# Kernel optimization log

Hardware: AMD Instinct MI355X
Metric: run time of the kernel (lower is better)

The kernel has to match this reference:

```python
import jax, jax.numpy as jnp
import numpy as np

B, S, D, H = 4, 2048, 1024, 16
DEPTH = D // H  # 64


def setup_inputs() -> dict:
    key = jax.random.key(0)
    ks = jax.random.split(key, 11)
    scale = 1.0 / np.sqrt(D)
    inp = {
        "v": jax.random.normal(ks[0], (B, S, D), jnp.float32),
        "k": jax.random.normal(ks[1], (B, S, D), jnp.float32),
        "q": jax.random.normal(ks[2], (B, S, D), jnp.float32),
        # causal mask: 1.0 where attention is disallowed (strict upper triangle)
        "mask": jnp.triu(jnp.ones((S, S), jnp.float32), k=1)[None, None, :, :],
        "wq": jax.random.normal(ks[3], (D, D), jnp.float32) * scale,
        "bq": jnp.zeros((D,), jnp.float32),
        "wk": jax.random.normal(ks[4], (D, D), jnp.float32) * scale,
        "bk": jnp.zeros((D,), jnp.float32),
        "wv": jax.random.normal(ks[5], (D, D), jnp.float32) * scale,
        "bv": jnp.zeros((D,), jnp.float32),
        "wo": jax.random.normal(ks[6], (D, D), jnp.float32) * scale,
        "bo": jnp.zeros((D,), jnp.float32),
    }
    return inp


def _split_heads(x):
    # [B, S, D] -> [B, H, S, depth]
    b, s, _ = x.shape
    return x.reshape(b, s, H, DEPTH).transpose(0, 2, 1, 3)


def reference(v, k, q, mask, wq, bq, wk, bk, wv, bv, wo, bo):
    qh = _split_heads(q @ wq + bq)  # [B,H,S,depth]
    kh = _split_heads(k @ wk + bk)
    vh = _split_heads(v @ wv + bv)

    logits = jnp.einsum("bhqd,bhkd->bhqk", qh, kh) / jnp.sqrt(
        jnp.asarray(DEPTH, jnp.float32)
    )
    logits = logits + mask * -1e9
    attn = jax.nn.softmax(logits, axis=-1)  # [B,H,S,S]
    out = jnp.einsum("bhqk,bhkd->bhqd", attn, vh)
    out = out.transpose(0, 2, 1, 3).reshape(q.shape[0], -1, D)  # [B,S,D]
    return out @ wo + bo
```

## Files before the change

### kernel.cpp

```cpp
#include <hip/hip_runtime.h>

typedef _Float16 f16;
typedef _Float16 half8 __attribute__((ext_vector_type(8)));
typedef _Float16 half4v __attribute__((ext_vector_type(4)));
typedef float f32x4 __attribute__((ext_vector_type(4)));

__device__ __forceinline__ void gl_lds16(const void* g, void* l) {
    __builtin_amdgcn_global_load_lds((const __attribute__((address_space(1))) void*)g,
                                     (__attribute__((address_space(3))) void*)l, 16, 0, 0);
}

__device__ __forceinline__ void prep_w_body(const float* __restrict__ W, f16* __restrict__ Wt)
{
    __shared__ float t[64][65];
    const int tid = threadIdx.x;
    const int tk = blockIdx.x * 64, tn = blockIdx.y * 64;
    const int rr = tid >> 4, cc = (tid & 15) * 4;
    #pragma unroll
    for (int j = 0; j < 4; ++j) {
        float4 v = *(const float4*)(W + (size_t)(tk + rr + j * 16) * 1024 + tn + cc);
        t[rr + j * 16][cc] = v.x; t[rr + j * 16][cc + 1] = v.y;
        t[rr + j * 16][cc + 2] = v.z; t[rr + j * 16][cc + 3] = v.w;
    }
    __syncthreads();
    const int n = tid >> 2, kc = (tid & 3) * 16;
    f16 o[16];
    #pragma unroll
    for (int j = 0; j < 16; ++j) o[j] = (f16)t[kc + j][n];
    f16* dst = Wt + (size_t)(tn + n) * 1024 + tk + kc;
    *(uint4*)dst = *(uint4*)o;
    *(uint4*)(dst + 8) = *(uint4*)(o + 8);
}

__global__ __launch_bounds__(256) void prep_w1(const float* __restrict__ W, f16* __restrict__ Wt)
{ prep_w_body(W, Wt); }

__global__ __launch_bounds__(256) void prep_w3(const float* __restrict__ w0,
    const float* __restrict__ w1, const float* __restrict__ w2, f16* __restrict__ Wt)
{
    const int z = blockIdx.z;
    const float* W = (z == 0) ? w0 : (z == 1) ? w1 : w2;
    prep_w_body(W, Wt + (size_t)z * 1024 * 1024);
}

template<int MODE>
__global__ __launch_bounds__(256, 2) void gemm_kernel(
    const void* __restrict__ Xv, const f16* __restrict__ Wt,
    const float* __restrict__ bias, void* __restrict__ outv)
{
    __shared__ __align__(16) f16 Bs[128 * 32];
    __shared__ __align__(16) f16 As[(MODE == 1) ? (128 * 32) : (128 * 64)];
    float* Asf = (float*)As;

    const int tid = threadIdx.x;
    const int lane = tid & 63;
    const int lane16 = lane & 15, quad = lane >> 4;
    const int wave = tid >> 6;
    const int wm = (wave >> 1) * 64, wn = (wave & 1) * 64;

    const int lin = blockIdx.x + 8 * blockIdx.y;
    const int xcd = lin & 7, t = lin >> 3;
    const int m0 = ((t >> 3) * 8 + xcd) * 128;
    const int n0 = (t & 7) * 128;

    const int wbase = tid & 192;
    const int l3 = lane16 & 7, l2 = lane16 & 3;

    f32x4 acc[4][4] = {};

    for (int k0 = 0; k0 < 1024; k0 += 32) {
        __syncthreads();
        #pragma unroll
        for (int i = 0; i < 2; ++i) {
            const int row = i * 64 + (tid >> 2);
            gl_lds16(Wt + (size_t)(n0 + row) * 1024 + k0 + (((tid & 3) ^ (row & 3)) * 8),
                     Bs + (size_t)(i * 256 + wbase) * 8);
        }
        if (MODE == 1) {
            const f16* Xh = (const f16*)Xv;
            #pragma unroll
            for (int i = 0; i < 2; ++i) {
                const int row = i * 64 + (tid >> 2);
                gl_lds16(Xh + (size_t)(m0 + row) * 1024 + k0 + (((tid & 3) ^ (row & 3)) * 8),
                         As + (size_t)(i * 256 + wbase) * 8);
            }
        } else {
            const float* Xf = (const float*)Xv;
            #pragma unroll
            for (int i = 0; i < 4; ++i) {
                const int row = i * 32 + (tid >> 3);
                gl_lds16(Xf + (size_t)(m0 + row) * 1024 + k0 + (((tid & 7) ^ (row & 7)) * 4),
                         Asf + (size_t)(i * 256 + wbase) * 4);
            }
        }
        __syncthreads();

        half8 af[4], bf[4];
        #pragma unroll
        for (int i = 0; i < 4; ++i) {
            const int row = wm + i * 16 + lane16;
            if (MODE == 1) {
                af[i] = *(const half8*)(As + row * 32 + ((quad ^ l2) * 8));
            } else {
                const float4 f0 = *(const float4*)(Asf + row * 32 + (((2 * quad)     ^ l3) * 4));
                const float4 f1 = *(const float4*)(Asf + row * 32 + (((2 * quad + 1) ^ l3) * 4));
                half8 h;
                h[0] = (f16)f0.x; h[1] = (f16)f0.y; h[2] = (f16)f0.z; h[3] = (f16)f0.w;
                h[4] = (f16)f1.x; h[5] = (f16)f1.y; h[6] = (f16)f1.z; h[7] = (f16)f1.w;
                af[i] = h;
            }
        }
        #pragma unroll
        for (int i = 0; i < 4; ++i) {
            const int row = wn + i * 16 + lane16;
            bf[i] = *(const half8*)(Bs + row * 32 + ((quad ^ l2) * 8));
        }
        #pragma unroll
        for (int mi = 0; mi < 4; ++mi)
            #pragma unroll
            for (int ni = 0; ni < 4; ++ni)
                acc[mi][ni] = __builtin_amdgcn_mfma_f32_16x16x32_f16(af[mi], bf[ni], acc[mi][ni], 0, 0, 0);
    }

    #pragma unroll
    for (int mi = 0; mi < 4; ++mi) {
        #pragma unroll
        for (int ni = 0; ni < 4; ++ni) {
            const int col = n0 + wn + ni * 16 + lane16;
            const float bval = bias[col];
            const int grow0 = m0 + wm + mi * 16 + quad * 4;
            if (MODE == 2) {
                const int b = grow0 >> 11, s0 = grow0 & 2047;
                const int h = col >> 6, d = col & 63;
                half4v p;
                #pragma unroll
                for (int r = 0; r < 4; ++r) p[r] = (f16)(acc[mi][ni][r] + bval);
                *(half4v*)((f16*)outv + (((size_t)b * 16 + h) * 64 + d) * 2048 + s0) = p;
            } else if (MODE == 0) {
                #pragma unroll
                for (int r = 0; r < 4; ++r) {
                    const int grow = grow0 + r;
                    const int b = grow >> 11, s = grow & 2047;
                    const int h = col >> 6, d = col & 63;
                    ((f16*)outv)[(((size_t)b * 16 + h) * 2048 + s) * 64 + d] = (f16)(acc[mi][ni][r] + bval);
                }
            } else {
                #pragma unroll
                for (int r = 0; r < 4; ++r)
                    ((float*)outv)[(size_t)(grow0 + r) * 1024 + col] = acc[mi][ni][r] + bval;
            }
        }
    }
}

__global__ __launch_bounds__(256, 2) void attn_kernel(
    const f16* __restrict__ qh, const f16* __restrict__ kh,
    const f16* __restrict__ vt, f16* __restrict__ at)
{
    __shared__ __align__(16) f16 Ks[64 * 64];
    __shared__ __align__(16) f16 Vts[64 * 64];
    __shared__ __align__(16) f16 Pt[4][32 * 72];

    const int tid = threadIdx.x;
    const int lane = tid & 63, wave = tid >> 6;
    const int lane16 = lane & 15, quad = lane >> 4;
    const int wbase = tid & 192;
    const int l3 = lane16 & 7;

    const int lin = blockIdx.x + 8 * blockIdx.y;
    const int xcd = lin & 7, t = lin >> 3;
    const int bh = xcd + 8 * (t & 7);
    const int bx = t >> 3;
    const int b = bh >> 4, h = bh & 15;

    const f16* qp = qh + (size_t)bh * 2048 * 64;
    const f16* kp = kh + (size_t)bh * 2048 * 64;
    const f16* vtp = vt + (size_t)bh * 64 * 2048;
    f16* Ptw = Pt[wave];

    for (int pass = 0; pass < 2; ++pass) {
        const int qb = 128 * (pass == 0 ? (15 - bx) : bx);
        const int qrow0 = qb + wave * 32;

        half8 aq[2][2];
        #pragma unroll
        for (int mt = 0; mt < 2; ++mt)
            #pragma unroll
            for (int c = 0; c < 2; ++c)
                aq[mt][c] = *(const half8*)(qp + (size_t)(qrow0 + mt * 16 + lane16) * 64 + c * 32 + quad * 8);

        f32x4 o[4][2] = {};
        float lp[2] = {0.0f, 0.0f};
        const int ntiles = qb / 64 + 2;
        const int qmax = qrow0 + 31;

        for (int kt = 0; kt < ntiles; ++kt) {
            const int k0 = kt * 64;
            __syncthreads();
            #pragma unroll
            for (int i = 0; i < 2; ++i) {
                const int row = i * 32 + (tid >> 3);
                const int sw = ((tid & 7) ^ (row & 7)) * 8;
                gl_lds16(kp + (size_t)(k0 + row) * 64 + sw, Ks + (size_t)(i * 256 + wbase) * 8);
                gl_lds16(vtp + (size_t)row * 2048 + k0 + sw, Vts + (size_t)(i * 256 + wbase) * 8);
            }
            __syncthreads();

            if (k0 <= qmax) {
                f32x4 sT[4][2];
                #pragma unroll
                for (int sub = 0; sub < 4; ++sub) {
                    const int kr = sub * 16 + lane16;
                    const half8 ak0 = *(const half8*)(Ks + kr * 64 + ((quad ^ l3) * 8));
                    const half8 ak1 = *(const half8*)(Ks + kr * 64 + (((4 + quad) ^ l3) * 8));
                    #pragma unroll
                    for (int mt = 0; mt < 2; ++mt) {
                        f32x4 z = {};
                        z = __builtin_amdgcn_mfma_f32_16x16x32_f16(ak0, aq[mt][0], z, 0, 0, 0);
                        z = __builtin_amdgcn_mfma_f32_16x16x32_f16(ak1, aq[mt][1], z, 0, 0, 0);
                        sT[sub][mt] = z;
                    }
                }
                const bool needmask = (k0 + 63 > qrow0);
                if (needmask) {
                    #pragma unroll
                    for (int sub = 0; sub < 4; ++sub)
                        #pragma unroll
                        for (int mt = 0; mt < 2; ++mt)
                            #pragma unroll
                            for (int r = 0; r < 4; ++r) {
                                const int key = k0 + sub * 16 + quad * 4 + r;
                                const int qi = qrow0 + mt * 16 + lane16;
                                if (key > qi) sT[sub][mt][r] = -1e30f;
                            }
                }
                #pragma unroll
                for (int sub = 0; sub < 4; ++sub)
                    #pragma unroll
                    for (int mt = 0; mt < 2; ++mt) {
                        #pragma unroll
                        for (int r = 0; r < 4; ++r) {
                            const float p = __expf(fmaf(sT[sub][mt][r], 0.125f, -4.0f));
                            sT[sub][mt][r] = p;
                            lp[mt] += p;
                        }
                        *(half4v*)(Ptw + (mt * 16 + lane16) * 72 + sub * 16 + quad * 4) =
                            (half4v){(f16)sT[sub][mt][0], (f16)sT[sub][mt][1],
                                     (f16)sT[sub][mt][2], (f16)sT[sub][mt][3]};
                    }
                asm volatile("" ::: "memory");

                half8 bp[2][2];
                #pragma unroll
                for (int mt = 0; mt < 2; ++mt)
                    #pragma unroll
                    for (int c = 0; c < 2; ++c)
                        bp[c][mt] = *(const half8*)(Ptw + (mt * 16 + lane16) * 72 + c * 32 + quad * 8);
                #pragma unroll
                for (int nt = 0; nt < 4; ++nt) {
                    const int dr = nt * 16 + lane16;
                    const half8 av0 = *(const half8*)(Vts + dr * 64 + ((quad ^ l3) * 8));
                    const half8 av1 = *(const half8*)(Vts + dr * 64 + (((4 + quad) ^ l3) * 8));
                    #pragma unroll
                    for (int mt = 0; mt < 2; ++mt) {
                        o[nt][mt] = __builtin_amdgcn_mfma_f32_16x16x32_f16(av0, bp[0][mt], o[nt][mt], 0, 0, 0);
                        o[nt][mt] = __builtin_amdgcn_mfma_f32_16x16x32_f16(av1, bp[1][mt], o[nt][mt], 0, 0, 0);
                    }
                }
            }
        }

        #pragma unroll
        for (int mt = 0; mt < 2; ++mt) {
            float red = lp[mt];
            red += __shfl_xor(red, 16);
            red += __shfl_xor(red, 32);
            const float inv = 1.0f / red;
            const int srow = qrow0 + mt * 16 + lane16;
            f16* dst = at + ((size_t)b * 2048 + srow) * 1024 + h * 64 + quad * 4;
            #pragma unroll
            for (int nt = 0; nt < 4; ++nt) {
                half4v p;
                #pragma unroll
                for (int r = 0; r < 4; ++r) p[r] = (f16)(o[nt][mt][r] * inv);
                *(half4v*)(dst + nt * 16) = p;
            }
        }
    }
}

extern "C" void kernel_launch(void* const* d_in, const int* in_sizes, int n_in,
                              void* d_out, int out_size, void* d_ws, size_t ws_size,
                              hipStream_t stream)
{
    const float* v  = (const float*)d_in[0];
    const float* k  = (const float*)d_in[1];
    const float* q  = (const float*)d_in[2];
    const float* wq = (const float*)d_in[4];
    const float* bq = (const float*)d_in[5];
    const float* wk = (const float*)d_in[6];
    const float* bk = (const float*)d_in[7];
    const float* wv = (const float*)d_in[8];
    const float* bv = (const float*)d_in[9];
    const float* wo = (const float*)d_in[10];
    const float* bo = (const float*)d_in[11];

    f16* qh = (f16*)d_ws;
    f16* kh = qh + (size_t)8 * 1024 * 1024;
    f16* vt = kh + (size_t)8 * 1024 * 1024;
    f16* at = vt + (size_t)8 * 1024 * 1024;

    f16* wqT = (f16*)d_out;
    f16* wkT = wqT + (size_t)1024 * 1024;
    f16* wvT = wkT + (size_t)1024 * 1024;
    f16* woT = qh;

    prep_w3<<<dim3(16, 16, 3), 256, 0, stream>>>(wq, wk, wv, wqT);

    dim3 g(8, 64);
    gemm_kernel<0><<<g, 256, 0, stream>>>(q, wqT, bq, qh);
    gemm_kernel<0><<<g, 256, 0, stream>>>(k, wkT, bk, kh);
    gemm_kernel<2><<<g, 256, 0, stream>>>(v, wvT, bv, vt);

    attn_kernel<<<dim3(8, 64), 256, 0, stream>>>(qh, kh, vt, at);

    prep_w1<<<dim3(16, 16), 256, 0, stream>>>(wo, woT);
    gemm_kernel<1><<<g, 256, 0, stream>>>(at, woT, bo, d_out);
}
```

Before: 369.7 us.

## Pre-convert activations to fp16 and store Q/K projections in row-major layout

Adds a standalone fp32-to-fp16 conversion kernel for q, k and v, so the projection GEMMs load fp16 activations. This halves the A-tile LDS footprint and removes the per-fragment conversion from the inner loop. The Q/K projection epilogue now writes plain row-major [B,S,D] instead of the head-split layout, and the attention kernel reads with a 1024 stride. The trade-off is three extra full-tensor read/write passes plus kernel launches, in exchange for a simpler, lighter GEMM inner loop and coalesced epilogue stores.

After: 338.0 us. -8.6%, faster.

```diff
diff --git a/kernel.cpp b/kernel.cpp
--- a/kernel.cpp
+++ b/kernel.cpp
@@ -8,6 +8,17 @@
 __device__ __forceinline__ void gl_lds16(const void* g, void* l) {
     __builtin_amdgcn_global_load_lds((const __attribute__((address_space(1))) void*)g,
                                      (__attribute__((address_space(3))) void*)l, 16, 0, 0);
+}
+
+__global__ __launch_bounds__(256) void cvt_f32_f16(const float* __restrict__ x, f16* __restrict__ y)
+{
+    const size_t i = ((size_t)blockIdx.x * 256 + threadIdx.x) * 8;
+    const float4 a = *(const float4*)(x + i);
+    const float4 b = *(const float4*)(x + i + 4);
+    half8 h;
+    h[0] = (f16)a.x; h[1] = (f16)a.y; h[2] = (f16)a.z; h[3] = (f16)a.w;
+    h[4] = (f16)b.x; h[5] = (f16)b.y; h[6] = (f16)b.z; h[7] = (f16)b.w;
+    *(half8*)(y + i) = h;
 }
 
 __device__ __forceinline__ void prep_w_body(const float* __restrict__ W, f16* __restrict__ Wt)
@@ -43,14 +54,13 @@
     prep_w_body(W, Wt + (size_t)z * 1024 * 1024);
 }
 
-template<int MODE>
+template<int OUT>
 __global__ __launch_bounds__(256, 2) void gemm_kernel(
-    const void* __restrict__ Xv, const f16* __restrict__ Wt,
+    const f16* __restrict__ X, const f16* __restrict__ Wt,
     const float* __restrict__ bias, void* __restrict__ outv)
 {
+    __shared__ __align__(16) f16 As[128 * 32];
     __shared__ __align__(16) f16 Bs[128 * 32];
-    __shared__ __align__(16) f16 As[(MODE == 1) ? (128 * 32) : (128 * 64)];
-    float* Asf = (float*)As;
 
     const int tid = threadIdx.x;
     const int lane = tid & 63;
@@ -64,7 +74,7 @@
     const int n0 = (t & 7) * 128;
 
     const int wbase = tid & 192;
-    const int l3 = lane16 & 7, l2 = lane16 & 3;
+    const int l2 = lane16 & 3;
 
     f32x4 acc[4][4] = {};
 
@@ -73,48 +83,19 @@
         #pragma unroll
         for (int i = 0; i < 2; ++i) {
             const int row = i * 64 + (tid >> 2);
-            gl_lds16(Wt + (size_t)(n0 + row) * 1024 + k0 + (((tid & 3) ^ (row & 3)) * 8),
-                     Bs + (size_t)(i * 256 + wbase) * 8);
-        }
-        if (MODE == 1) {
-            const f16* Xh = (const f16*)Xv;
-            #pragma unroll
-            for (int i = 0; i < 2; ++i) {
-                const int row = i * 64 + (tid >> 2);
-                gl_lds16(Xh + (size_t)(m0 + row) * 1024 + k0 + (((tid & 3) ^ (row & 3)) * 8),
-                         As + (size_t)(i * 256 + wbase) * 8);
-            }
-        } else {
-            const float* Xf = (const float*)Xv;
-            #pragma unroll
-            for (int i = 0; i < 4; ++i) {
-                const int row = i * 32 + (tid >> 3);
-                gl_lds16(Xf + (size_t)(m0 + row) * 1024 + k0 + (((tid & 7) ^ (row & 7)) * 4),
-                         Asf + (size_t)(i * 256 + wbase) * 4);
-            }
+            const int sw = ((tid & 3) ^ (row & 3)) * 8;
+            gl_lds16(Wt + (size_t)(n0 + row) * 1024 + k0 + sw, Bs + (size_t)(i * 256 + wbase) * 8);
+            gl_lds16(X  + (size_t)(m0 + row) * 1024 + k0 + sw, As + (size_t)(i * 256 + wbase) * 8);
         }
         __syncthreads();
 
         half8 af[4], bf[4];
         #pragma unroll
-        for (int i = 0; i < 4; ++i) {
-            const int row = wm + i * 16 + lane16;
-            if (MODE == 1) {
-                af[i] = *(const half8*)(As + row * 32 + ((quad ^ l2) * 8));
-            } else {
-                const float4 f0 = *(const float4*)(Asf + row * 32 + (((2 * quad)     ^ l3) * 4));
-                const float4 f1 = *(const float4*)(Asf + row * 32 + (((2 * quad + 1) ^ l3) * 4));
-                half8 h;
-                h[0] = (f16)f0.x; h[1] = (f16)f0.y; h[2] = (f16)f0.z; h[3] = (f16)f0.w;
-                h[4] = (f16)f1.x; h[5] = (f16)f1.y; h[6] = (f16)f1.z; h[7] = (f16)f1.w;
-                af[i] = h;
-            }
-        }
-        #pragma unroll
-        for (int i = 0; i < 4; ++i) {
-            const int row = wn + i * 16 + lane16;
-            bf[i] = *(const half8*)(Bs + row * 32 + ((quad ^ l2) * 8));
-        }
+        for (int i = 0; i < 4; ++i)
+            af[i] = *(const half8*)(As + (wm + i * 16 + lane16) * 32 + ((quad ^ l2) * 8));
+        #pragma unroll
+        for (int i = 0; i < 4; ++i)
+            bf[i] = *(const half8*)(Bs + (wn + i * 16 + lane16) * 32 + ((quad ^ l2) * 8));
         #pragma unroll
         for (int mi = 0; mi < 4; ++mi)
             #pragma unroll
@@ -129,21 +110,17 @@
             const int col = n0 + wn + ni * 16 + lane16;
             const float bval = bias[col];
             const int grow0 = m0 + wm + mi * 16 + quad * 4;
-            if (MODE == 2) {
+            if (OUT == 2) {
                 const int b = grow0 >> 11, s0 = grow0 & 2047;
                 const int h = col >> 6, d = col & 63;
                 half4v p;
                 #pragma unroll
                 for (int r = 0; r < 4; ++r) p[r] = (f16)(acc[mi][ni][r] + bval);
                 *(half4v*)((f16*)outv + (((size_t)b * 16 + h) * 64 + d) * 2048 + s0) = p;
-            } else if (MODE == 0) {
-                #pragma unroll
-                for (int r = 0; r < 4; ++r) {
-                    const int grow = grow0 + r;
-                    const int b = grow >> 11, s = grow & 2047;
-                    const int h = col >> 6, d = col & 63;
-                    ((f16*)outv)[(((size_t)b * 16 + h) * 2048 + s) * 64 + d] = (f16)(acc[mi][ni][r] + bval);
-                }
+            } else if (OUT == 0) {
+                #pragma unroll
+                for (int r = 0; r < 4; ++r)
+                    ((f16*)outv)[(size_t)(grow0 + r) * 1024 + col] = (f16)(acc[mi][ni][r] + bval);
             } else {
                 #pragma unroll
                 for (int r = 0; r < 4; ++r)
@@ -173,8 +150,8 @@
     const int bx = t >> 3;
     const int b = bh >> 4, h = bh & 15;
 
-    const f16* qp = qh + (size_t)bh * 2048 * 64;
-    const f16* kp = kh + (size_t)bh * 2048 * 64;
+    const f16* qp = qh + (size_t)b * 2048 * 1024 + h * 64;
+    const f16* kp = kh + (size_t)b * 2048 * 1024 + h * 64;
     const f16* vtp = vt + (size_t)bh * 64 * 2048;
     f16* Ptw = Pt[wave];
 
@@ -187,7 +164,7 @@
         for (int mt = 0; mt < 2; ++mt)
             #pragma unroll
             for (int c = 0; c < 2; ++c)
-                aq[mt][c] = *(const half8*)(qp + (size_t)(qrow0 + mt * 16 + lane16) * 64 + c * 32 + quad * 8);
+                aq[mt][c] = *(const half8*)(qp + (size_t)(qrow0 + mt * 16 + lane16) * 1024 + c * 32 + quad * 8);
 
         f32x4 o[4][2] = {};
         float lp[2] = {0.0f, 0.0f};
@@ -201,7 +178,7 @@
             for (int i = 0; i < 2; ++i) {
                 const int row = i * 32 + (tid >> 3);
                 const int sw = ((tid & 7) ^ (row & 7)) * 8;
-                gl_lds16(kp + (size_t)(k0 + row) * 64 + sw, Ks + (size_t)(i * 256 + wbase) * 8);
+                gl_lds16(kp + (size_t)(k0 + row) * 1024 + sw, Ks + (size_t)(i * 256 + wbase) * 8);
                 gl_lds16(vtp + (size_t)row * 2048 + k0 + sw, Vts + (size_t)(i * 256 + wbase) * 8);
             }
             __syncthreads();
@@ -310,17 +287,22 @@
     f16* vt = kh + (size_t)8 * 1024 * 1024;
     f16* at = vt + (size_t)8 * 1024 * 1024;
 
-    f16* wqT = (f16*)d_out;
-    f16* wkT = wqT + (size_t)1024 * 1024;
-    f16* wvT = wkT + (size_t)1024 * 1024;
+    f16* wT = (f16*)d_out;
+    f16* wqT = wT;
+    f16* wkT = wT + (size_t)1024 * 1024;
+    f16* wvT = wT + (size_t)2 * 1024 * 1024;
+    f16* xf  = wT + (size_t)3 * 1024 * 1024;
     f16* woT = qh;
 
-    prep_w3<<<dim3(16, 16, 3), 256, 0, stream>>>(wq, wk, wv, wqT);
+    prep_w3<<<dim3(16, 16, 3), 256, 0, stream>>>(wq, wk, wv, wT);
 
     dim3 g(8, 64);
-    gemm_kernel<0><<<g, 256, 0, stream>>>(q, wqT, bq, qh);
-    gemm_kernel<0><<<g, 256, 0, stream>>>(k, wkT, bk, kh);
-    gemm_kernel<2><<<g, 256, 0, stream>>>(v, wvT, bv, vt);
+    cvt_f32_f16<<<4096, 256, 0, stream>>>(q, xf);
+    gemm_kernel<0><<<g, 256, 0, stream>>>(xf, wqT, bq, qh);
+    cvt_f32_f16<<<4096, 256, 0, stream>>>(k, xf);
+    gemm_kernel<0><<<g, 256, 0, stream>>>(xf, wkT, bk, kh);
+    cvt_f32_f16<<<4096, 256, 0, stream>>>(v, xf);
+    gemm_kernel<2><<<g, 256, 0, stream>>>(xf, wvT, bv, vt);
 
     attn_kernel<<<dim3(8, 64), 256, 0, stream>>>(qh, kh, vt, at);
 
```
